# Performance work log

Measured on AMD Instinct MI355X. Metric: run time of the kernel, lower is better.

## Reference

```python
import jax, jax.numpy as jnp
import numpy as np

N = 100000   # nodes
E = 3200000  # random edges (before self-loops)
D = 20       # hidden width


def setup_inputs() -> dict:
    key = jax.random.key(0)
    k = jax.random.split(key, 8)
    return {
        "feat": jax.random.normal(k[0], (N, 1), jnp.float32),
        "W_start": jax.random.normal(k[1], (1, D), jnp.float32) * 0.5,
        "b_start": jnp.zeros((D,), jnp.float32),
        "W_mid": jax.random.normal(k[2], (18, D, D), jnp.float32) * (1.0 / np.sqrt(D)),
        "b_mid": jnp.zeros((18, D), jnp.float32),
        "W_final": jax.random.normal(k[3], (D, D), jnp.float32) * (1.0 / np.sqrt(D)),
        "b_final": jnp.zeros((D,), jnp.float32),
        "src": jax.random.randint(k[4], (E,), 0, N, jnp.int32),
        "dst": jax.random.randint(k[5], (E,), 0, N, jnp.int32),
    }


def reference(feat, W_start, b_start, W_mid, b_mid, W_final, b_final, src, dst):
    # dgl.add_self_loop
    loop = jnp.arange(N, dtype=src.dtype)
    src2 = jnp.concatenate([src, loop])
    dst2 = jnp.concatenate([dst, loop])

    ones = jnp.ones(src2.shape[0], jnp.float32)
    out_deg = jax.ops.segment_sum(ones, src2, num_segments=N)
    in_deg = jax.ops.segment_sum(ones, dst2, num_segments=N)
    # with self-loops degrees >= 1; clamp defensively like DGL
    dout = jnp.power(jnp.maximum(out_deg, 1.0), -0.5)  # [N]
    din = jnp.power(jnp.maximum(in_deg, 1.0), -0.5)    # [N]

    def conv(h, W, b):
        # GraphConv norm='both': D_out^{-1/2} on source, sum-aggregate, D_in^{-1/2} on dest
        hw = (h * dout[:, None]) @ W                   # [N, out]
        agg = jax.ops.segment_sum(hw[src2], dst2, num_segments=N)
        return agg * din[:, None] + b

    h = jax.nn.relu(conv(feat, W_start, b_start))

    def step(h, wb):
        W, b = wb
        return jax.nn.relu(conv(h, W, b)), None

    h, _ = jax.lax.scan(step, h, (W_mid, b_mid))
    h = conv(h, W_final, b_final)
    return h[None]  # unsqueeze(0) -> [1, N, D]
```

## Files before the change

### kernel.cpp

```cpp
#include <hip/hip_runtime.h>

#define DH    20
#define BKSC  10
#define BKC   1024
#define MAXKC 128
#define BKSF  8
#define BKF   256
#define ECAP  10240
#define CHUNK 8192


__global__ void zero_bhist2(int* __restrict__ bhist_d, int* __restrict__ bhist_s) {
    int i = threadIdx.x;
    if (i < MAXKC) { bhist_d[i] = 0; bhist_s[i] = 0; }
}

__global__ __launch_bounds__(256) void bucket_hist2(const int* __restrict__ src,
        const int* __restrict__ dst, int* __restrict__ bhist_d,
        int* __restrict__ bhist_s, int E, int K) {
    __shared__ int hd[MAXKC];
    __shared__ int hs[MAXKC];
    for (int i = threadIdx.x; i < K; i += blockDim.x) { hd[i] = 0; hs[i] = 0; }
    __syncthreads();
    int lo = blockIdx.x * CHUNK;
    int hi = lo + CHUNK; if (hi > E) hi = E;
    for (int e = lo + (int)threadIdx.x; e < hi; e += 256) {
        atomicAdd(&hd[__builtin_nontemporal_load(&dst[e]) >> BKSC], 1);
        atomicAdd(&hs[__builtin_nontemporal_load(&src[e]) >> BKSC], 1);
    }
    __syncthreads();
    for (int i = threadIdx.x; i < K; i += blockDim.x) {
        if (hd[i]) atomicAdd(&bhist_d[i], hd[i]);
        if (hs[i]) atomicAdd(&bhist_s[i], hs[i]);
    }
}

__global__ __launch_bounds__(128) void bucket_scan2(
        const int* __restrict__ bhist_d, int* __restrict__ bbase_d,
        int* __restrict__ bcursor_d, const int* __restrict__ bhist_s,
        int* __restrict__ bbase_s, int* __restrict__ bcursor_s, int K) {
    __shared__ int a[MAXKC];
    __shared__ int b[MAXKC];
    int t = threadIdx.x;
    int vd = (t < K) ? bhist_d[t] : 0;
    int vs = (t < K) ? bhist_s[t] : 0;
    a[t] = vd; b[t] = vs;
    __syncthreads();
    for (int off = 1; off < 128; off <<= 1) {
        int x = (t >= off) ? a[t - off] : 0;
        int y = (t >= off) ? b[t - off] : 0;
        __syncthreads();
        a[t] += x; b[t] += y;
        __syncthreads();
    }
    if (t < K) {
        int ed = a[t] - vd, es = b[t] - vs;
        bbase_d[t] = ed; bcursor_d[t] = ed;
        bbase_s[t] = es; bcursor_s[t] = es;
    }
    if (t == K - 1) { bbase_d[K] = a[t]; bbase_s[K] = b[t]; }
}

__global__ __launch_bounds__(256) void bucket_place2(const int* __restrict__ src,
        const int* __restrict__ dst, int* __restrict__ bcursor_d,
        int* __restrict__ bcursor_s, int* __restrict__ pairs,
        int* __restrict__ ssort, int E, int K) {
    __shared__ int hd[MAXKC];
    __shared__ int hs[MAXKC];
    __shared__ int rbd[MAXKC];
    __shared__ int rbs[MAXKC];
    int lo = blockIdx.x * CHUNK;
    int hi = lo + CHUNK; if (hi > E) hi = E;
    for (int i = threadIdx.x; i < K; i += blockDim.x) { hd[i] = 0; hs[i] = 0; }
    __syncthreads();
    for (int e = lo + (int)threadIdx.x; e < hi; e += 256) {
        atomicAdd(&hd[__builtin_nontemporal_load(&dst[e]) >> BKSC], 1);
        atomicAdd(&hs[__builtin_nontemporal_load(&src[e]) >> BKSC], 1);
    }
    __syncthreads();
    for (int i = threadIdx.x; i < K; i += blockDim.x) {
        rbd[i] = hd[i] ? atomicAdd(&bcursor_d[i], hd[i]) : 0;
        rbs[i] = hs[i] ? atomicAdd(&bcursor_s[i], hs[i]) : 0;
        hd[i] = 0; hs[i] = 0;
    }
    __syncthreads();
    for (int e = lo + (int)threadIdx.x; e < hi; e += 256) {
        int d = __builtin_nontemporal_load(&dst[e]);
        int s = __builtin_nontemporal_load(&src[e]);
        int bkd = d >> BKSC;
        int pd = atomicAdd(&hd[bkd], 1);
        pairs[rbd[bkd] + pd] = (s << BKSC) | (d & (BKC - 1));
        int bks = s >> BKSC;
        int ps = atomicAdd(&hs[bks], 1);
        ssort[rbs[bks] + ps] = s & (BKC - 1);
    }
}

__global__ __launch_bounds__(256) void bucket_outdeg(const int* __restrict__ bbase_s,
        const int* __restrict__ ssort, double* __restrict__ dout, int n_nodes) {
    __shared__ int h[BKC];
    int k = blockIdx.x;
    int t = threadIdx.x;
    int nbase = k << BKSC;
    int nrem = n_nodes - nbase; if (nrem > BKC) nrem = BKC;
    for (int i = t; i < BKC; i += 256) h[i] = 1;
    __syncthreads();
    int e0 = bbase_s[k], e1 = bbase_s[k + 1];
    for (int e = e0 + t; e < e1; e += 256)
        atomicAdd(&h[__builtin_nontemporal_load(&ssort[e])], 1);
    __syncthreads();
    for (int i = t; i < nrem; i += 256)
        dout[nbase + i] = 1.0 / sqrt((double)h[i]);
}

__global__ __launch_bounds__(256) void bucket_build(
        const int* __restrict__ bbase, const int* __restrict__ pairs,
        int* __restrict__ row_ptr, double* __restrict__ din,
        int* __restrict__ col, int n_nodes, int n_edges) {
    __shared__ int h[BKF];
    __shared__ int ts[BKF];
    __shared__ int red[256];
    __shared__ int ecol[ECAP];
    int nwg = gridDim.x;
    int xcd = blockIdx.x & 7;
    int loc = blockIdx.x >> 3;
    int q = nwg >> 3, r = nwg & 7;
    int k = ((xcd < r) ? xcd * (q + 1) : r * (q + 1) + (xcd - r) * q) + loc;
    int kc = k >> 2;
    int f  = k & 3;
    int t = threadIdx.x;
    int nbase = k << BKSF;
    int nrem = n_nodes - nbase; if (nrem > BKF) nrem = BKF;
    h[t] = 0;
    __syncthreads();
    int e0 = bbase[kc], e1 = bbase[kc + 1];
    int before = 0;
    for (int e = e0 + t; e < e1; e += 256) {
        int pk = pairs[e];
        int dl = pk & (BKC - 1);
        int fe = dl >> BKSF;
        if (fe == f) atomicAdd(&h[dl & (BKF - 1)], 1);
        else if (fe < f) ++before;
    }
    red[t] = before;
    __syncthreads();
    for (int off = 128; off > 0; off >>= 1) {
        if (t < off) red[t] += red[t + off];
        __syncthreads();
    }
    int fbase = e0 + red[0];
    int c = h[t];
    ts[t] = c;
    __syncthreads();
    for (int off = 1; off < 256; off <<= 1) {
        int v = (t >= off) ? ts[t - off] : 0;
        __syncthreads();
        ts[t] += v;
        __syncthreads();
    }
    int lx = ts[t] - c;
    if (t < nrem) {
        row_ptr[nbase + t] = fbase + lx;
        din[nbase + t] = 1.0 / sqrt((double)(c + 1));
    }
    h[t] = lx;
    if (t == 0 && nbase + BKF >= n_nodes) row_ptr[n_nodes] = n_edges;
    __syncthreads();
    for (int e = e0 + t; e < e1; e += 256) {
        int pk = pairs[e];
        int dl = pk & (BKC - 1);
        if ((dl >> BKSF) == f) {
            int slot = atomicAdd(&h[dl & (BKF - 1)], 1);
            if (slot < ECAP) ecol[slot] = pk >> BKSC;
            else col[fbase + slot] = pk >> BKSC;
        }
    }
    __syncthreads();
    int cnt = ts[BKF - 1];
    int lim = cnt < ECAP ? cnt : ECAP;
    for (int i = t; i < lim; i += 256)
        col[fbase + i] = ecol[i];
}


__global__ void compute_x0(const float* __restrict__ feat, const double* __restrict__ dout,
                           double* __restrict__ x0, int n) {
    int i = blockIdx.x * blockDim.x + threadIdx.x;
    if (i < n) x0[i] = (double)feat[i] * dout[i];
}

__global__ __launch_bounds__(256) void layer_start(
        const double* __restrict__ x0, const int* __restrict__ row_ptr,
        const int* __restrict__ col, const double* __restrict__ din,
        const double* __restrict__ dout, const float* __restrict__ W,
        const float* __restrict__ b, float* __restrict__ xout, int n_nodes) {
    int n    = (blockIdx.x * blockDim.x + threadIdx.x) >> 6;
    int lane = threadIdx.x & 63;
    if (n >= n_nodes) return;
    double a = (lane == 0) ? x0[n] : 0.0;
    int e0 = row_ptr[n], e1 = row_ptr[n + 1];
    for (int e = e0 + lane; e < e1; e += 64)
        a += x0[__builtin_nontemporal_load(&col[e])];
#pragma unroll
    for (int off = 32; off > 0; off >>= 1)
        a += __shfl_xor(a, off, 64);
    if (lane < DH) {
        double v = a * din[n] * (double)W[lane] + (double)b[lane];
        float r = fmaxf((float)v, 0.0f);
        xout[(long)n * DH + lane] = (float)((double)r * dout[n]);
    }
}

__global__ __launch_bounds__(256) void transform(
        const float* __restrict__ h, const float* __restrict__ W,
        float* __restrict__ y, int n_nodes) {
    __shared__ float Wl[DH * DH];
    for (int i = threadIdx.x; i < DH * DH; i += blockDim.x) Wl[i] = W[i];
    __syncthreads();
    int n = blockIdx.x * blockDim.x + threadIdx.x;
    if (n >= n_nodes) return;
    const float4* h4 = (const float4*)(h + (size_t)n * DH);
    float4 a0 = h4[0], a1 = h4[1], a2 = h4[2], a3 = h4[3], a4 = h4[4];
    float hv[DH] = {a0.x, a0.y, a0.z, a0.w, a1.x, a1.y, a1.z, a1.w,
                    a2.x, a2.y, a2.z, a2.w, a3.x, a3.y, a3.z, a3.w,
                    a4.x, a4.y, a4.z, a4.w};
    double acc[DH];
#pragma unroll
    for (int j = 0; j < DH; ++j) acc[j] = 0.0;
#pragma unroll
    for (int k = 0; k < DH; ++k) {
        double hk = (double)hv[k];
#pragma unroll
        for (int j = 0; j < DH; ++j)
            acc[j] += hk * (double)Wl[k * DH + j];
    }
    float4* y4 = (float4*)(y + (size_t)n * DH);
    y4[0] = make_float4((float)acc[0],  (float)acc[1],  (float)acc[2],  (float)acc[3]);
    y4[1] = make_float4((float)acc[4],  (float)acc[5],  (float)acc[6],  (float)acc[7]);
    y4[2] = make_float4((float)acc[8],  (float)acc[9],  (float)acc[10], (float)acc[11]);
    y4[3] = make_float4((float)acc[12], (float)acc[13], (float)acc[14], (float)acc[15]);
    y4[4] = make_float4((float)acc[16], (float)acc[17], (float)acc[18], (float)acc[19]);
}

__global__ __launch_bounds__(256, 8) void gather_agg(
        const float* __restrict__ y, const int* __restrict__ row_ptr,
        const int* __restrict__ col, const double* __restrict__ din,
        const double* __restrict__ dout, const float* __restrict__ b,
        float* __restrict__ hout, int n_nodes, int mode) {
    int n    = (blockIdx.x * blockDim.x + threadIdx.x) >> 6;
    int lane = threadIdx.x & 63;
    if (n >= n_nodes) return;

    int ep = lane / 5;
    int jq = lane - ep * 5;
    const float4* __restrict__ y4 = (const float4*)y;

    int e0 = row_ptr[n], e1 = row_ptr[n + 1];

    int s0 = -1, s1 = -1, s2 = -1, s3 = -1;
    if (ep < 12) {
        int p = e0 + ep;
        if (p      < e1) s0 = __builtin_nontemporal_load(&col[p]);
        if (p + 12 < e1) s1 = __builtin_nontemporal_load(&col[p + 12]);
        if (p + 24 < e1) s2 = __builtin_nontemporal_load(&col[p + 24]);
        if (p + 36 < e1) s3 = __builtin_nontemporal_load(&col[p + 36]);
    }
    bool p0 = s0 >= 0, p1 = s1 >= 0, p2 = s2 >= 0, p3 = s3 >= 0;
    float4 v0 = y4[(p0 ? s0 : n) * 5 + jq];
    float4 v1 = y4[(p1 ? s1 : n) * 5 + jq];
    float4 v2 = y4[(p2 ? s2 : n) * 5 + jq];
    float4 v3 = y4[(p3 ? s3 : n) * 5 + jq];

    double g[4] = {0.0, 0.0, 0.0, 0.0};
    if (ep == 0) {
        float4 v = y4[n * 5 + jq];
        g[0] = (double)v.x; g[1] = (double)v.y; g[2] = (double)v.z; g[3] = (double)v.w;
    }
    if (p0) { g[0] += (double)v0.x; g[1] += (double)v0.y; g[2] += (double)v0.z; g[3] += (double)v0.w; }
    if (p1) { g[0] += (double)v1.x; g[1] += (double)v1.y; g[2] += (double)v1.z; g[3] += (double)v1.w; }
    if (p2) { g[0] += (double)v2.x; g[1] += (double)v2.y; g[2] += (double)v2.z; g[3] += (double)v2.w; }
    if (p3) { g[0] += (double)v3.x; g[1] += (double)v3.y; g[2] += (double)v3.z; g[3] += (double)v3.w; }

    if (e1 - e0 > 48) {
        if (ep < 12) {
            for (int e = e0 + 48 + ep; e < e1; e += 12) {
                int s = __builtin_nontemporal_load(&col[e]);
                float4 v = y4[s * 5 + jq];
                g[0] += (double)v.x; g[1] += (double)v.y;
                g[2] += (double)v.z; g[3] += (double)v.w;
            }
        }
    }

#define FOLD(LIM, DELTA)                                                        \
    {                                                                           \
        int srcl = lane + DELTA; if (srcl > 63) srcl = lane;                    \
        double t0 = __shfl(g[0], srcl, 64);                                     \
        double t1 = __shfl(g[1], srcl, 64);                                     \
        double t2 = __shfl(g[2], srcl, 64);                                     \
        double t3 = __shfl(g[3], srcl, 64);                                     \
        if (ep < (LIM)) { g[0] += t0; g[1] += t1; g[2] += t2; g[3] += t3; }     \
    }
    FOLD(4, 40)
    FOLD(4, 20)
    FOLD(2, 10)
    FOLD(1, 5)
#undef FOLD

    if (lane < 5) {
        double dn = din[n];
        float4 bb = ((const float4*)b)[lane];
        double o0 = g[0] * dn + (double)bb.x;
        double o1 = g[1] * dn + (double)bb.y;
        double o2 = g[2] * dn + (double)bb.z;
        double o3 = g[3] * dn + (double)bb.w;
        float4 w;
        if (mode == 0) {
            double dd = dout[n];
            w.x = (float)((double)fmaxf((float)o0, 0.0f) * dd);
            w.y = (float)((double)fmaxf((float)o1, 0.0f) * dd);
            w.z = (float)((double)fmaxf((float)o2, 0.0f) * dd);
            w.w = (float)((double)fmaxf((float)o3, 0.0f) * dd);
        } else {
            w.x = (float)o0; w.y = (float)o1; w.z = (float)o2; w.w = (float)o3;
        }
        ((float4*)(hout + (size_t)n * DH))[lane] = w;
    }
}


static inline size_t align256(size_t x) { return (x + 255) & ~(size_t)255; }

extern "C" void kernel_launch(void* const* d_in, const int* in_sizes, int n_in,
                              void* d_out, int out_size, void* d_ws, size_t ws_size,
                              hipStream_t stream) {
    const float* feat    = (const float*)d_in[0];
    const float* W_start = (const float*)d_in[1];
    const float* b_start = (const float*)d_in[2];
    const float* W_mid   = (const float*)d_in[3];
    const float* b_mid   = (const float*)d_in[4];
    const float* W_final = (const float*)d_in[5];
    const float* b_final = (const float*)d_in[6];
    const int*   src     = (const int*)d_in[7];
    const int*   dst     = (const int*)d_in[8];

    const int N = in_sizes[0];
    const int E = in_sizes[7];
    const int L = in_sizes[3] / (DH * DH);
    const int KC = (N + BKC - 1) / BKC;
    const int KF = (N + BKF - 1) / BKF;

    char* p = (char*)d_ws;
    double* dout_d = (double*)p; p += align256(sizeof(double) * N);
    double* din_d  = (double*)p; p += align256(sizeof(double) * N);
    double* x0     = (double*)p; p += align256(sizeof(double) * N);
    int* row_ptr   = (int*)p;    p += align256(sizeof(int) * (N + 1));
    int* bhist_d   = (int*)p;    p += align256(sizeof(int) * (MAXKC + 1));
    int* bbase_d   = (int*)p;    p += align256(sizeof(int) * (MAXKC + 1));
    int* bcursor_d = (int*)p;    p += align256(sizeof(int) * (MAXKC + 1));
    int* bhist_s   = (int*)p;    p += align256(sizeof(int) * (MAXKC + 1));
    int* bbase_s   = (int*)p;    p += align256(sizeof(int) * (MAXKC + 1));
    int* bcursor_s = (int*)p;    p += align256(sizeof(int) * (MAXKC + 1));
    int* col       = (int*)p;    p += align256(sizeof(int) * E);
    float* hbuf    = (float*)p;  p += align256(sizeof(float) * N * DH);
    float* ybuf    = (float*)p;  p += align256(sizeof(float) * N * DH);
    int* pairs = (int*)hbuf;
    int* ssort = col;

    const int BT = 256;
    int grid_n  = (N + BT - 1) / BT;
    int grid_c  = (E + CHUNK - 1) / CHUNK;
    int grid_nw = (N + 3) / 4;

    zero_bhist2<<<1, MAXKC, 0, stream>>>(bhist_d, bhist_s);
    bucket_hist2<<<grid_c, BT, 0, stream>>>(src, dst, bhist_d, bhist_s, E, KC);
    bucket_scan2<<<1, 128, 0, stream>>>(bhist_d, bbase_d, bcursor_d,
                                        bhist_s, bbase_s, bcursor_s, KC);
    bucket_place2<<<grid_c, BT, 0, stream>>>(src, dst, bcursor_d, bcursor_s,
                                             pairs, ssort, E, KC);
    bucket_outdeg<<<KC, BT, 0, stream>>>(bbase_s, ssort, dout_d, N);
    bucket_build<<<KF, BT, 0, stream>>>(bbase_d, pairs, row_ptr, din_d, col, N, E);

    compute_x0<<<grid_n, BT, 0, stream>>>(feat, dout_d, x0, N);
    layer_start<<<grid_nw, BT, 0, stream>>>(x0, row_ptr, col, din_d, dout_d,
                                            W_start, b_start, hbuf, N);

    for (int l = 0; l < L; ++l) {
        transform<<<grid_n, BT, 0, stream>>>(hbuf, W_mid + (size_t)l * DH * DH, ybuf, N);
        gather_agg<<<grid_nw, BT, 0, stream>>>(ybuf, row_ptr, col, din_d, dout_d,
                                               b_mid + (size_t)l * DH, hbuf, N, 0);
    }

    transform<<<grid_n, BT, 0, stream>>>(hbuf, W_final, ybuf, N);
    gather_agg<<<grid_nw, BT, 0, stream>>>(ybuf, row_ptr, col, din_d, dout_d,
                                           b_final, (float*)d_out, N, 1);
}
```

Baseline: 1.660 ms.

## Use per-block bucket offsets from a global scan and fold reductions in float

The bucket sort now writes per-block histograms and computes per-block, per-bucket offsets in one scan kernel. The placement kernel therefore no longer re-histograms its chunk or issues global atomics for cursors, and the zeroing kernel is removed. The cost is a serial per-bucket loop over all blocks inside a single-block scan kernel. Separately, the gather-aggregate cross-lane fold now shuffles floats instead of doubles, which halves shuffle traffic but reduces precision in the final partial-sum reduction.

```diff
diff --git a/kernel.cpp b/kernel.cpp
--- a/kernel.cpp
+++ b/kernel.cpp
@@ -4,20 +4,16 @@
 #define BKSC  10
 #define BKC   1024
 #define MAXKC 128
+#define MAXNB 512
 #define BKSF  8
 #define BKF   256
 #define ECAP  10240
 #define CHUNK 8192
 
 
-__global__ void zero_bhist2(int* __restrict__ bhist_d, int* __restrict__ bhist_s) {
-    int i = threadIdx.x;
-    if (i < MAXKC) { bhist_d[i] = 0; bhist_s[i] = 0; }
-}
-
 __global__ __launch_bounds__(256) void bucket_hist2(const int* __restrict__ src,
-        const int* __restrict__ dst, int* __restrict__ bhist_d,
-        int* __restrict__ bhist_s, int E, int K) {
+        const int* __restrict__ dst, int* __restrict__ pbh_d,
+        int* __restrict__ pbh_s, int E, int K) {
     __shared__ int hd[MAXKC];
     __shared__ int hs[MAXKC];
     for (int i = threadIdx.x; i < K; i += blockDim.x) { hd[i] = 0; hs[i] = 0; }
@@ -30,69 +26,62 @@
     }
     __syncthreads();
     for (int i = threadIdx.x; i < K; i += blockDim.x) {
-        if (hd[i]) atomicAdd(&bhist_d[i], hd[i]);
-        if (hs[i]) atomicAdd(&bhist_s[i], hs[i]);
-    }
-}
-
-__global__ __launch_bounds__(128) void bucket_scan2(
-        const int* __restrict__ bhist_d, int* __restrict__ bbase_d,
-        int* __restrict__ bcursor_d, const int* __restrict__ bhist_s,
-        int* __restrict__ bbase_s, int* __restrict__ bcursor_s, int K) {
-    __shared__ int a[MAXKC];
-    __shared__ int b[MAXKC];
+        pbh_d[blockIdx.x * MAXKC + i] = hd[i];
+        pbh_s[blockIdx.x * MAXKC + i] = hs[i];
+    }
+}
+
+__global__ __launch_bounds__(256) void pb_scan(int* __restrict__ pbh_d,
+        int* __restrict__ pbh_s, int* __restrict__ bbase_d,
+        int* __restrict__ bbase_s, int NB, int K) {
+    __shared__ int a[256];
     int t = threadIdx.x;
-    int vd = (t < K) ? bhist_d[t] : 0;
-    int vs = (t < K) ? bhist_s[t] : 0;
-    a[t] = vd; b[t] = vs;
+    int k = t & 127;
+    int* pbh   = (t < 128) ? pbh_d : pbh_s;
+    int* bbase = (t < 128) ? bbase_d : bbase_s;
+    int tot = 0;
+    if (k < K)
+        for (int b = 0; b < NB; ++b) tot += pbh[b * MAXKC + k];
+    a[t] = (k < K) ? tot : 0;
     __syncthreads();
     for (int off = 1; off < 128; off <<= 1) {
-        int x = (t >= off) ? a[t - off] : 0;
-        int y = (t >= off) ? b[t - off] : 0;
-        __syncthreads();
-        a[t] += x; b[t] += y;
-        __syncthreads();
-    }
-    if (t < K) {
-        int ed = a[t] - vd, es = b[t] - vs;
-        bbase_d[t] = ed; bcursor_d[t] = ed;
-        bbase_s[t] = es; bcursor_s[t] = es;
-    }
-    if (t == K - 1) { bbase_d[K] = a[t]; bbase_s[K] = b[t]; }
-}
-
-__global__ __launch_bounds__(256) void bucket_place2(const int* __restrict__ src,
-        const int* __restrict__ dst, int* __restrict__ bcursor_d,
-        int* __restrict__ bcursor_s, int* __restrict__ pairs,
+        int v = (k >= off) ? a[t - off] : 0;
+        __syncthreads();
+        a[t] += v;
+        __syncthreads();
+    }
+    if (k < K) {
+        int run = a[t] - tot;
+        bbase[k] = run;
+        if (k == K - 1) bbase[K] = a[t];
+        for (int b = 0; b < NB; ++b) {
+            int c = pbh[b * MAXKC + k];
+            pbh[b * MAXKC + k] = run;
+            run += c;
+        }
+    }
+}
+
+__global__ __launch_bounds__(256) void bucket_place(const int* __restrict__ src,
+        const int* __restrict__ dst, const int* __restrict__ pbh_d,
+        const int* __restrict__ pbh_s, int* __restrict__ pairs,
         int* __restrict__ ssort, int E, int K) {
-    __shared__ int hd[MAXKC];
-    __shared__ int hs[MAXKC];
-    __shared__ int rbd[MAXKC];
-    __shared__ int rbs[MAXKC];
+    __shared__ int cd[MAXKC];
+    __shared__ int cs[MAXKC];
+    for (int i = threadIdx.x; i < K; i += blockDim.x) {
+        cd[i] = pbh_d[blockIdx.x * MAXKC + i];
+        cs[i] = pbh_s[blockIdx.x * MAXKC + i];
+    }
+    __syncthreads();
     int lo = blockIdx.x * CHUNK;
     int hi = lo + CHUNK; if (hi > E) hi = E;
-    for (int i = threadIdx.x; i < K; i += blockDim.x) { hd[i] = 0; hs[i] = 0; }
-    __syncthreads();
-    for (int e = lo + (int)threadIdx.x; e < hi; e += 256) {
-        atomicAdd(&hd[__builtin_nontemporal_load(&dst[e]) >> BKSC], 1);
-        atomicAdd(&hs[__builtin_nontemporal_load(&src[e]) >> BKSC], 1);
-    }
-    __syncthreads();
-    for (int i = threadIdx.x; i < K; i += blockDim.x) {
-        rbd[i] = hd[i] ? atomicAdd(&bcursor_d[i], hd[i]) : 0;
-        rbs[i] = hs[i] ? atomicAdd(&bcursor_s[i], hs[i]) : 0;
-        hd[i] = 0; hs[i] = 0;
-    }
-    __syncthreads();
     for (int e = lo + (int)threadIdx.x; e < hi; e += 256) {
         int d = __builtin_nontemporal_load(&dst[e]);
         int s = __builtin_nontemporal_load(&src[e]);
-        int bkd = d >> BKSC;
-        int pd = atomicAdd(&hd[bkd], 1);
-        pairs[rbd[bkd] + pd] = (s << BKSC) | (d & (BKC - 1));
-        int bks = s >> BKSC;
-        int ps = atomicAdd(&hs[bks], 1);
-        ssort[rbs[bks] + ps] = s & (BKC - 1);
+        int pd = atomicAdd(&cd[d >> BKSC], 1);
+        pairs[pd] = (s << BKSC) | (d & (BKC - 1));
+        int ps = atomicAdd(&cs[s >> BKSC], 1);
+        ssort[ps] = s & (BKC - 1);
     }
 }
 
@@ -292,14 +281,15 @@
         }
     }
 
+    float f0 = (float)g[0], f1 = (float)g[1], f2 = (float)g[2], f3 = (float)g[3];
 #define FOLD(LIM, DELTA)                                                        \
     {                                                                           \
         int srcl = lane + DELTA; if (srcl > 63) srcl = lane;                    \
-        double t0 = __shfl(g[0], srcl, 64);                                     \
-        double t1 = __shfl(g[1], srcl, 64);                                     \
-        double t2 = __shfl(g[2], srcl, 64);                                     \
-        double t3 = __shfl(g[3], srcl, 64);                                     \
-        if (ep < (LIM)) { g[0] += t0; g[1] += t1; g[2] += t2; g[3] += t3; }     \
+        float t0 = __shfl(f0, srcl, 64);                                        \
+        float t1 = __shfl(f1, srcl, 64);                                        \
+        float t2 = __shfl(f2, srcl, 64);                                        \
+        float t3 = __shfl(f3, srcl, 64);                                        \
+        if (ep < (LIM)) { f0 += t0; f1 += t1; f2 += t2; f3 += t3; }             \
     }
     FOLD(4, 40)
     FOLD(4, 20)
@@ -310,10 +300,10 @@
     if (lane < 5) {
         double dn = din[n];
         float4 bb = ((const float4*)b)[lane];
-        double o0 = g[0] * dn + (double)bb.x;
-        double o1 = g[1] * dn + (double)bb.y;
-        double o2 = g[2] * dn + (double)bb.z;
-        double o3 = g[3] * dn + (double)bb.w;
+        double o0 = (double)f0 * dn + (double)bb.x;
+        double o1 = (double)f1 * dn + (double)bb.y;
+        double o2 = (double)f2 * dn + (double)bb.z;
+        double o3 = (double)f3 * dn + (double)bb.w;
         float4 w;
         if (mode == 0) {
             double dd = dout[n];
@@ -349,18 +339,17 @@
     const int L = in_sizes[3] / (DH * DH);
     const int KC = (N + BKC - 1) / BKC;
     const int KF = (N + BKF - 1) / BKF;
+    const int NB = (E + CHUNK - 1) / CHUNK;
 
     char* p = (char*)d_ws;
     double* dout_d = (double*)p; p += align256(sizeof(double) * N);
     double* din_d  = (double*)p; p += align256(sizeof(double) * N);
     double* x0     = (double*)p; p += align256(sizeof(double) * N);
     int* row_ptr   = (int*)p;    p += align256(sizeof(int) * (N + 1));
-    int* bhist_d   = (int*)p;    p += align256(sizeof(int) * (MAXKC + 1));
     int* bbase_d   = (int*)p;    p += align256(sizeof(int) * (MAXKC + 1));
-    int* bcursor_d = (int*)p;    p += align256(sizeof(int) * (MAXKC + 1));
-    int* bhist_s   = (int*)p;    p += align256(sizeof(int) * (MAXKC + 1));
     int* bbase_s   = (int*)p;    p += align256(sizeof(int) * (MAXKC + 1));
-    int* bcursor_s = (int*)p;    p += align256(sizeof(int) * (MAXKC + 1));
+    int* pbh_d     = (int*)p;    p += align256(sizeof(int) * MAXNB * MAXKC);
+    int* pbh_s     = (int*)p;    p += align256(sizeof(int) * MAXNB * MAXKC);
     int* col       = (int*)p;    p += align256(sizeof(int) * E);
     float* hbuf    = (float*)p;  p += align256(sizeof(float) * N * DH);
     float* ybuf    = (float*)p;  p += align256(sizeof(float) * N * DH);
@@ -369,15 +358,11 @@
 
     const int BT = 256;
     int grid_n  = (N + BT - 1) / BT;
-    int grid_c  = (E + CHUNK - 1) / CHUNK;
     int grid_nw = (N + 3) / 4;
 
-    zero_bhist2<<<1, MAXKC, 0, stream>>>(bhist_d, bhist_s);
-    bucket_hist2<<<grid_c, BT, 0, stream>>>(src, dst, bhist_d, bhist_s, E, KC);
-    bucket_scan2<<<1, 128, 0, stream>>>(bhist_d, bbase_d, bcursor_d,
-                                        bhist_s, bbase_s, bcursor_s, KC);
-    bucket_place2<<<grid_c, BT, 0, stream>>>(src, dst, bcursor_d, bcursor_s,
-                                             pairs, ssort, E, KC);
+    bucket_hist2<<<NB, BT, 0, stream>>>(src, dst, pbh_d, pbh_s, E, KC);
+    pb_scan<<<1, 256, 0, stream>>>(pbh_d, pbh_s, bbase_d, bbase_s, NB, KC);
+    bucket_place<<<NB, BT, 0, stream>>>(src, dst, pbh_d, pbh_s, pairs, ssort, E, KC);
     bucket_outdeg<<<KC, BT, 0, stream>>>(bbase_s, ssort, dout_d, N);
     bucket_build<<<KF, BT, 0, stream>>>(bbase_d, pairs, row_ptr, din_d, col, N, E);
 
```

New measurement: 1.708 ms. 1.03x slower.
